# Kernel tuning notes

Hardware: AMD Instinct MI355X
Metric: run time of the kernel (lower is better)

Reference implementation:

```python
import jax, jax.numpy as jnp
import numpy as np
import math

B, S, H = 4, 2048, 1024
NE, NC, CD, OD = 4, 16, 64, 128  # num_experiments, num_exp_codes, exp_code_dim, outcome_dim
TAU, TEMP, EPS = 0.5, 0.07, 1e-5


def gelu(x):
    return jax.nn.gelu(x, approximate=False)


def layer_norm(x, g, b):
    m = x.mean(-1, keepdims=True)
    v = ((x - m) ** 2).mean(-1, keepdims=True)
    return (x - m) * jax.lax.rsqrt(v + EPS) * g + b


def setup_inputs() -> dict:
    key = jax.random.key(0)
    ks = jax.random.split(key, 24)
    lin = lambda k, i, o: jax.random.normal(k, (i, o), jnp.float32) * 0.02
    u = jax.random.uniform(ks[1], (B, NE, NC), minval=1e-6, maxval=1.0 - 1e-6)
    d = {
        "hidden_states": jax.random.normal(ks[0], (B, S, H), jnp.float32),
        "attention_mask": jnp.ones((B, S), jnp.int32),
        "gumbel_noise": -jnp.log(-jnp.log(u)),
        # context_pooler: Linear(H,H) + LayerNorm
        "cp_w": lin(ks[2], H, H), "cp_b": jnp.zeros(H), "cp_ln_g": jnp.ones(H), "cp_ln_b": jnp.zeros(H),
        # eph: Linear(H,H), Linear(H, NE*NC)
        "eph_w1": lin(ks[3], H, H), "eph_b1": jnp.zeros(H),
        "eph_w2": lin(ks[4], H, NE * NC), "eph_b2": jnp.zeros(NE * NC),
        "codebook": jax.random.normal(ks[5], (NC, CD), jnp.float32) * 0.02,
        # world_kernel: Linear(H+CD, 2H), Linear(2H, OD)
        "wk_w1": lin(ks[6], H + CD, 2 * H), "wk_b1": jnp.zeros(2 * H),
        "wk_w2": lin(ks[7], 2 * H, OD), "wk_b2": jnp.zeros(OD),
        "tp_w": lin(ks[8], H, OD),  # target_proj, no bias
        # film_proj: Linear(OD, 2H) + GELU
        "film_w": lin(ks[9], OD, 2 * H), "film_b": jnp.zeros(2 * H),
        "q_w": lin(ks[10], H, H), "q_b": jnp.zeros(H),
        "k_w": lin(ks[11], H, H), "k_b": jnp.zeros(H),
        "v_w": lin(ks[12], H, H), "v_b": jnp.zeros(H),
        "o_w": lin(ks[13], H, H), "o_b": jnp.zeros(H),
        "int_w": lin(ks[14], H, 4 * H), "int_b": jnp.zeros(4 * H),
        "out_w": lin(ks[15], 4 * H, H), "out_b": jnp.zeros(H),
        "ln_g": jnp.ones(H), "ln_b": jnp.zeros(H),
    }
    return d


def reference(hidden_states, attention_mask, gumbel_noise,
              cp_w, cp_b, cp_ln_g, cp_ln_b,
              eph_w1, eph_b1, eph_w2, eph_b2, codebook,
              wk_w1, wk_b1, wk_w2, wk_b2, tp_w, film_w, film_b,
              q_w, q_b, k_w, k_b, v_w, v_b, o_w, o_b,
              int_w, int_b, out_w, out_b, ln_g, ln_b):
    mask = attention_mask.astype(hidden_states.dtype)  # [B,S]
    # --- context pooling ---
    denom = mask.sum(1, keepdims=True) + 1e-8
    pooled = (hidden_states * mask[:, :, None]).sum(1) / denom  # [B,H]
    h_ctx = layer_norm(gelu(pooled @ cp_w + cp_b), cp_ln_g, cp_ln_b)
    # --- experiment proposal (gumbel-softmax, hard, tau=0.5) ---
    z_raw = gelu(h_ctx @ eph_w1 + eph_b1) @ eph_w2 + eph_b2
    z_logits = z_raw.reshape(B, NE, NC)
    y_soft = jax.nn.softmax((z_logits + gumbel_noise) / TAU, axis=-1)
    y_hard = jax.nn.one_hot(jnp.argmax(y_soft, -1), NC, dtype=y_soft.dtype)
    z_soft = y_hard - jax.lax.stop_gradient(y_soft) + y_soft  # straight-through
    z_codes = z_soft @ codebook  # [B,NE,CD]
    # --- world kernel ---
    h_rep = jnp.broadcast_to(h_ctx[:, None, :], (B, NE, H))
    h_wk = jnp.concatenate([h_rep, z_codes], -1)  # [B,NE,H+CD]
    outcome = gelu(h_wk @ wk_w1 + wk_b1) @ wk_w2 + wk_b2  # [B,NE,OD]
    # --- info gain (labels/plan_vector None branch) ---
    tv = h_ctx @ tp_w
    tv = tv / jnp.linalg.norm(tv, axis=-1, keepdims=True).clip(1e-12)
    on = outcome / jnp.linalg.norm(outcome, axis=-1, keepdims=True).clip(1e-12)
    info_gain = jnp.sum(on * tv[:, None, :], -1) / TEMP  # [B,NE]
    idx = jnp.argmax(info_gain, -1)  # [B]
    chosen = jnp.take_along_axis(outcome, idx[:, None, None], axis=1)[:, 0]  # [B,OD]
    # --- FiLM ---
    gb = gelu(chosen @ film_w + film_b)  # [B,2H]
    gamma, beta = gb[:, :H], gb[:, H:]
    fused = gamma[:, None, :] * hidden_states + beta[:, None, :]  # [B,S,H]
    # --- single-head attention ---
    q = fused @ q_w + q_b
    k = fused @ k_w + k_b
    v = fused @ v_w + v_b
    scores = jnp.einsum('bqd,bkd->bqk', q, k) / math.sqrt(H)
    scores = jnp.where(attention_mask[:, None, :] == 0, -jnp.inf, scores)
    attn = jax.nn.softmax(scores, axis=-1)
    attn_out = jnp.einsum('bqk,bkd->bqd', attn, v) @ o_w + o_b
    # --- FFN + residual + LN ---
    ff = gelu((attn_out + fused) @ int_w + int_b) @ out_w + out_b
    return layer_norm(ff + fused, ln_g, ln_b)
```

## Files before the change

### kernel.cpp

```cpp
#include <hip/hip_runtime.h>
#include <math.h>

#define DEVI __device__ __forceinline__

typedef unsigned short u16;
typedef __attribute__((ext_vector_type(4))) float f32x4;
typedef __attribute__((ext_vector_type(8))) short s16x8;
typedef __attribute__((ext_vector_type(4))) short s16x4;

constexpr int Bc = 4, Sc = 2048, Hc = 1024;
constexpr int NEc = 4, NCc = 16, CDc = 64, ODc = 128;
constexpr float TAUc = 0.5f, TEMPc = 0.07f, EPSc = 1e-5f;

DEVI float gelu_f(float x) { return 0.5f * x * (1.0f + erff(x * 0.7071067811865476f)); }

DEVI float bf2f(u16 u) { union { unsigned int i; float f; } v; v.i = ((unsigned int)u) << 16; return v.f; }
DEVI u16 f2bf(float f) {
  union { float f; unsigned int i; } v; v.f = f;
  unsigned int u = v.i;
  unsigned int r = (u + 0x7fffu + ((u >> 16) & 1u)) >> 16;
  return (u16)r;
}

DEVI float wred_sum(float v) {
  #pragma unroll
  for (int o = 32; o > 0; o >>= 1) v += __shfl_down(v, o);
  return v;
}
DEVI float wred_max(float v) {
  #pragma unroll
  for (int o = 32; o > 0; o >>= 1) v = fmaxf(v, __shfl_down(v, o));
  return v;
}

DEVI void gload16(const void* g, void* l) {
  __builtin_amdgcn_global_load_lds((const __attribute__((address_space(1))) void*)g,
                                   (__attribute__((address_space(3))) void*)l, 16, 0, 0);
}

template<int EPI>
__global__ __launch_bounds__(256, 3) void gemm_bt(
    const u16* __restrict__ A, long sAz, int lda,
    const u16* __restrict__ Bt, long sBz, int ldb,
    u16* __restrict__ C, long sCz, int ldc,
    const float* __restrict__ bias,
    const u16* __restrict__ resid, long sRz,
    float scale, int M, int N, int K)
{
  const int bz = blockIdx.z;
  A += (long)bz * sAz; Bt += (long)bz * sBz; C += (long)bz * sCz;
  if (EPI & 4) resid += (long)bz * sRz;

  const int nTn = N >> 7;
  const int tm = blockIdx.x / nTn, tn = blockIdx.x % nTn;
  const int tid = threadIdx.x;
  const int wid = tid >> 6, lane = tid & 63;
  const int wr = wid >> 1, wc = wid & 1;
  const int l15 = lane & 15, l4 = lane >> 4;

  __shared__ u16 As[128 * 32];
  __shared__ u16 Bs[128 * 32];

  f32x4 acc[4][4];
  #pragma unroll
  for (int i = 0; i < 4; ++i)
    #pragma unroll
    for (int j = 0; j < 4; ++j) acc[i][j] = f32x4{0.f, 0.f, 0.f, 0.f};

  const int srow = (wid << 5) + (lane >> 2);
  const int scol = (lane & 3) << 3;
  const u16* aS = A + (long)(tm * 128 + srow) * lda + scol;
  const u16* bS = Bt + (long)(tn * 128 + srow) * ldb + scol;
  const long aStep16 = (long)16 * lda;
  const long bStep16 = (long)16 * ldb;
  u16* aD = &As[wid * 32 * 32];
  u16* bD = &Bs[wid * 32 * 32];

  for (int k0 = 0; k0 < K; k0 += 32) {
    gload16(aS, aD);
    gload16(aS + aStep16, aD + 16 * 32);
    gload16(bS, bD);
    gload16(bS + bStep16, bD + 16 * 32);
    __syncthreads();
    s16x8 af[4], bfr[4];
    #pragma unroll
    for (int i = 0; i < 4; ++i) {
      const int row = (wr << 6) + (i << 4) + l15;
      af[i] = *(const s16x8*)&As[(row << 5) + (l4 << 3)];
    }
    #pragma unroll
    for (int j = 0; j < 4; ++j) {
      const int col = (wc << 6) + (j << 4) + l15;
      bfr[j] = *(const s16x8*)&Bs[(col << 5) + (l4 << 3)];
    }
    #pragma unroll
    for (int i = 0; i < 4; ++i)
      #pragma unroll
      for (int j = 0; j < 4; ++j)
        acc[i][j] = __builtin_amdgcn_mfma_f32_16x16x32_bf16(af[i], bfr[j], acc[i][j], 0, 0, 0);
    __syncthreads();
    aS += 32; bS += 32;
  }

  #pragma unroll
  for (int j = 0; j < 4; ++j) {
    const int col = tn * 128 + (wc << 6) + (j << 4) + l15;
    const float bv = (EPI & 1) ? bias[col] : 0.f;
    #pragma unroll
    for (int i = 0; i < 4; ++i) {
      const int row0 = tm * 128 + (wr << 6) + (i << 4) + (l4 << 2);
      float vv[4];
      #pragma unroll
      for (int r = 0; r < 4; ++r) {
        float v = acc[i][j][r] * scale + bv;
        if (EPI & 2) v = gelu_f(v);
        if (EPI & 4) v += bf2f(resid[(long)(row0 + r) * ldc + col]);
        vv[r] = v;
      }
      if (EPI & 8) {
        s16x4 pk = { (short)f2bf(vv[0]), (short)f2bf(vv[1]), (short)f2bf(vv[2]), (short)f2bf(vv[3]) };
        *(s16x4*)&C[(long)col * ldc + row0] = pk;
      } else {
        #pragma unroll
        for (int r = 0; r < 4; ++r) C[(long)(row0 + r) * ldc + col] = f2bf(vv[r]);
      }
    }
  }
}

__global__ void transpose_w_k(const float* __restrict__ in, u16* __restrict__ out, int K, int N) {
  __shared__ float t[32][33];
  const int n0 = blockIdx.x << 5, k0 = blockIdx.y << 5;
  const int tx = threadIdx.x, ty = threadIdx.y;
  #pragma unroll
  for (int i = 0; i < 32; i += 8)
    t[ty + i][tx] = in[(long)(k0 + ty + i) * N + n0 + tx];
  __syncthreads();
  #pragma unroll
  for (int i = 0; i < 32; i += 8)
    out[(long)(n0 + ty + i) * K + k0 + tx] = f2bf(t[tx][ty + i]);
}

__global__ void transpose_w4_k(const float* __restrict__ w0, const float* __restrict__ w1,
                               const float* __restrict__ w2, const float* __restrict__ w3,
                               u16* __restrict__ o0, u16* __restrict__ o1,
                               u16* __restrict__ o2, u16* __restrict__ o3) {
  const int z = blockIdx.z;
  const float* in = (z == 0) ? w0 : (z == 1) ? w1 : (z == 2) ? w2 : w3;
  u16* out = (z == 0) ? o0 : (z == 1) ? o1 : (z == 2) ? o2 : o3;
  __shared__ float t[32][33];
  const int n0 = blockIdx.x << 5, k0 = blockIdx.y << 5;
  const int tx = threadIdx.x, ty = threadIdx.y;
  #pragma unroll
  for (int i = 0; i < 32; i += 8)
    t[ty + i][tx] = in[(long)(k0 + ty + i) * Hc + n0 + tx];
  __syncthreads();
  #pragma unroll
  for (int i = 0; i < 32; i += 8)
    out[(long)(n0 + ty + i) * Hc + k0 + tx] = f2bf(t[tx][ty + i]);
}

__global__ void pool_partial_k(const float* __restrict__ hs, const int* __restrict__ mask,
                               float* __restrict__ part) {
  const int h = (blockIdx.x << 8) + threadIdx.x;
  const int c = blockIdx.y, b = blockIdx.z;
  const int s0 = c * (Sc / 16);
  float acc = 0.f;
  for (int i = 0; i < Sc / 16; ++i) {
    const int s = s0 + i;
    acc += hs[((long)b * Sc + s) * Hc + h] * (float)mask[b * Sc + s];
  }
  part[((b << 4) + c) * Hc + h] = acc;
}

__global__ void pool_final_k(const float* __restrict__ part, const int* __restrict__ mask,
                             float* __restrict__ pooled) {
  const int b = blockIdx.x;
  __shared__ float red[4];
  __shared__ float denom_s;
  float d = 0.f;
  for (int i = threadIdx.x; i < Sc; i += 256) d += (float)mask[b * Sc + i];
  d = wred_sum(d);
  if ((threadIdx.x & 63) == 0) red[threadIdx.x >> 6] = d;
  __syncthreads();
  if (threadIdx.x == 0) denom_s = red[0] + red[1] + red[2] + red[3] + 1e-8f;
  __syncthreads();
  const float inv = 1.f / denom_s;
  for (int h = threadIdx.x; h < Hc; h += 256) {
    float s = 0.f;
    #pragma unroll
    for (int c = 0; c < 16; ++c) s += part[((b << 4) + c) * Hc + h];
    pooled[b * Hc + h] = s * inv;
  }
}

template<int R>
__global__ void mrow_part_k(const float* __restrict__ in, const float* __restrict__ W,
                            float* __restrict__ part, int K, int N) {
  const int t = threadIdx.x;
  const int jj = t & 31;
  const int j = (blockIdx.x << 5) + jj;
  const int ks = t >> 5;
  const int nchunk = gridDim.y;
  const int Kc = K / (nchunk << 3);
  const int k0 = ((blockIdx.y << 3) + ks) * Kc;
  float acc[R];
  #pragma unroll
  for (int r = 0; r < R; ++r) acc[r] = 0.f;
  for (int k = k0; k < k0 + Kc; ++k) {
    const float wv = W[(long)k * N + j];
    #pragma unroll
    for (int r = 0; r < R; ++r) acc[r] = fmaf(in[r * K + k], wv, acc[r]);
  }
  __shared__ float sm[8][R][32];
  #pragma unroll
  for (int r = 0; r < R; ++r) sm[ks][r][jj] = acc[r];
  __syncthreads();
  for (int idx = t; idx < R * 32; idx += 256) {
    const int r = idx >> 5, j2 = idx & 31;
    float s = 0.f;
    #pragma unroll
    for (int q = 0; q < 8; ++q) s += sm[q][r][j2];
    part[(long)(blockIdx.y * R + r) * N + (blockIdx.x << 5) + j2] = s;
  }
}

template<bool GELU>
__global__ void mrow_reduce_k(const float* __restrict__ part, const float* __restrict__ bias,
                              float* __restrict__ out, int N, int R, int nchunk) {
  const int idx = (blockIdx.x << 8) + threadIdx.x;
  if (idx >= R * N) return;
  const int r = idx / N, j = idx - r * N;
  float s = 0.f;
  for (int c = 0; c < nchunk; ++c) s += part[(long)(c * R + r) * N + j];
  if (bias) s += bias[j];
  if (GELU) s = gelu_f(s);
  out[(long)r * N + j] = s;
}

__global__ void ln_rows_k(float* __restrict__ x, const float* __restrict__ g,
                          const float* __restrict__ b) {
  const long base = (long)blockIdx.x * Hc;
  __shared__ float red[4];
  float v[4]; float s = 0.f;
  #pragma unroll
  for (int i = 0; i < 4; ++i) { v[i] = x[base + threadIdx.x + (i << 8)]; s += v[i]; }
  s = wred_sum(s);
  if ((threadIdx.x & 63) == 0) red[threadIdx.x >> 6] = s;
  __syncthreads();
  const float mean = (red[0] + red[1] + red[2] + red[3]) * (1.f / Hc);
  float q = 0.f;
  #pragma unroll
  for (int i = 0; i < 4; ++i) { const float d2 = v[i] - mean; q += d2 * d2; }
  __syncthreads();
  q = wred_sum(q);
  if ((threadIdx.x & 63) == 0) red[threadIdx.x >> 6] = q;
  __syncthreads();
  const float var = (red[0] + red[1] + red[2] + red[3]) * (1.f / Hc);
  const float inv = rsqrtf(var + EPSc);
  #pragma unroll
  for (int i = 0; i < 4; ++i) {
    const int col = threadIdx.x + (i << 8);
    x[base + col] = (v[i] - mean) * inv * g[col] + b[col];
  }
}

__global__ void gumbel_k(const float* __restrict__ z, const float* __restrict__ gn,
                         const float* __restrict__ cb, float* __restrict__ zcodes) {
  const int b = blockIdx.x, t = threadIdx.x;
  if (t >= NEc) return;
  const float* zp = z + b * (NEc * NCc) + t * NCc;
  const float* gp = gn + (b * NEc + t) * NCc;
  int best = 0; float bv = -3.4e38f;
  for (int c2 = 0; c2 < NCc; ++c2) {
    const float val = (zp[c2] + gp[c2]) * (1.f / TAUc);
    if (val > bv) { bv = val; best = c2; }
  }
  for (int d2 = 0; d2 < CDc; ++d2)
    zcodes[(b * NEc + t) * CDc + d2] = cb[best * CDc + d2];
}

__global__ void build_hwk_k(const float* __restrict__ hctx, const float* __restrict__ zcodes,
                            float* __restrict__ hwk) {
  const int r = blockIdx.x;
  const int b = r >> 2;
  for (int i = threadIdx.x; i < Hc + CDc; i += 256)
    hwk[r * (Hc + CDc) + i] = (i < Hc) ? hctx[b * Hc + i] : zcodes[r * CDc + (i - Hc)];
}

__global__ void select_k(const float* __restrict__ tv, const float* __restrict__ outc,
                         float* __restrict__ chosen) {
  const int b = blockIdx.x, t = threadIdx.x;
  __shared__ float red[2];
  __shared__ float ig[NEc];
  __shared__ int bestIdx;
  const float x = tv[b * ODc + t];
  float ss = wred_sum(x * x);
  if ((t & 63) == 0) red[t >> 6] = ss;
  __syncthreads();
  float nrm = fmaxf(sqrtf(red[0] + red[1]), 1e-12f);
  const float tvn = x / nrm;
  __syncthreads();
  for (int ne = 0; ne < NEc; ++ne) {
    const float o = outc[(b * NEc + ne) * ODc + t];
    float a = wred_sum(o * o);
    float d2 = wred_sum(o * tvn);
    if ((t & 63) == 0) red[t >> 6] = a;
    __syncthreads();
    const float no = sqrtf(red[0] + red[1]);
    __syncthreads();
    if ((t & 63) == 0) red[t >> 6] = d2;
    __syncthreads();
    const float dd = red[0] + red[1];
    if (t == 0) ig[ne] = dd / fmaxf(no, 1e-12f) * (1.f / TEMPc);
    __syncthreads();
  }
  if (t == 0) {
    int bi = 0; float bvv = ig[0];
    for (int ne = 1; ne < NEc; ++ne) if (ig[ne] > bvv) { bvv = ig[ne]; bi = ne; }
    bestIdx = bi;
  }
  __syncthreads();
  chosen[b * ODc + t] = outc[(b * NEc + bestIdx) * ODc + t];
}

__global__ void fuse_k(const float* __restrict__ hs, const float* __restrict__ gb,
                       u16* __restrict__ fused) {
  const long i = (((long)blockIdx.x << 8) + threadIdx.x) << 2;
  const int h = (int)(i & (Hc - 1));
  const int b = (int)(i >> 21);
  const float4 xv = *(const float4*)(hs + i);
  const float* gp = gb + b * 2048;
  s16x4 pk = { (short)f2bf(fmaf(gp[h + 0], xv.x, gp[Hc + h + 0])),
               (short)f2bf(fmaf(gp[h + 1], xv.y, gp[Hc + h + 1])),
               (short)f2bf(fmaf(gp[h + 2], xv.z, gp[Hc + h + 2])),
               (short)f2bf(fmaf(gp[h + 3], xv.w, gp[Hc + h + 3])) };
  *(s16x4*)(fused + i) = pk;
}

__global__ void softmax_k(u16* __restrict__ sc, const int* __restrict__ mask) {
  const long base = (long)blockIdx.x * Sc;
  const int b = blockIdx.x / Sc;
  __shared__ float red[4];
  float x[8];
  float mx = -3.0e38f;
  #pragma unroll
  for (int i = 0; i < 8; ++i) {
    const int col = threadIdx.x + (i << 8);
    float v = bf2f(sc[base + col]);
    if (mask[b * Sc + col] == 0) v = -3.0e38f;
    x[i] = v;
    mx = fmaxf(mx, v);
  }
  mx = wred_max(mx);
  if ((threadIdx.x & 63) == 0) red[threadIdx.x >> 6] = mx;
  __syncthreads();
  mx = fmaxf(fmaxf(red[0], red[1]), fmaxf(red[2], red[3]));
  float sum = 0.f;
  #pragma unroll
  for (int i = 0; i < 8; ++i) { x[i] = __expf(x[i] - mx); sum += x[i]; }
  __syncthreads();
  sum = wred_sum(sum);
  if ((threadIdx.x & 63) == 0) red[threadIdx.x >> 6] = sum;
  __syncthreads();
  const float inv = 1.f / (red[0] + red[1] + red[2] + red[3]);
  #pragma unroll
  for (int i = 0; i < 8; ++i)
    sc[base + threadIdx.x + (i << 8)] = f2bf(x[i] * inv);
}

__global__ void final_ln_k(const u16* __restrict__ ff, const u16* __restrict__ fused,
                           const float* __restrict__ g, const float* __restrict__ b,
                           float* __restrict__ out) {
  const long base = (long)blockIdx.x * Hc;
  __shared__ float red[4];
  float v[4]; float s = 0.f;
  #pragma unroll
  for (int i = 0; i < 4; ++i) {
    const int col = threadIdx.x + (i << 8);
    v[i] = bf2f(ff[base + col]) + bf2f(fused[base + col]);
    s += v[i];
  }
  s = wred_sum(s);
  if ((threadIdx.x & 63) == 0) red[threadIdx.x >> 6] = s;
  __syncthreads();
  const float mean = (red[0] + red[1] + red[2] + red[3]) * (1.f / Hc);
  float q = 0.f;
  #pragma unroll
  for (int i = 0; i < 4; ++i) { const float d2 = v[i] - mean; q += d2 * d2; }
  __syncthreads();
  q = wred_sum(q);
  if ((threadIdx.x & 63) == 0) red[threadIdx.x >> 6] = q;
  __syncthreads();
  const float var = (red[0] + red[1] + red[2] + red[3]) * (1.f / Hc);
  const float inv = rsqrtf(var + EPSc);
  #pragma unroll
  for (int i = 0; i < 4; ++i) {
    const int col = threadIdx.x + (i << 8);
    out[base + col] = (v[i] - mean) * inv * g[col] + b[col];
  }
}

extern "C" void kernel_launch(void* const* d_in, const int* in_sizes, int n_in,
                              void* d_out, int out_size, void* d_ws, size_t ws_size,
                              hipStream_t stream) {
  const float* hs       = (const float*)d_in[0];
  const int*   amask    = (const int*)d_in[1];
  const float* gn       = (const float*)d_in[2];
  const float* cp_w     = (const float*)d_in[3];
  const float* cp_b     = (const float*)d_in[4];
  const float* cp_ln_g  = (const float*)d_in[5];
  const float* cp_ln_b  = (const float*)d_in[6];
  const float* eph_w1   = (const float*)d_in[7];
  const float* eph_b1   = (const float*)d_in[8];
  const float* eph_w2   = (const float*)d_in[9];
  const float* eph_b2   = (const float*)d_in[10];
  const float* codebook = (const float*)d_in[11];
  const float* wk_w1    = (const float*)d_in[12];
  const float* wk_b1    = (const float*)d_in[13];
  const float* wk_w2    = (const float*)d_in[14];
  const float* wk_b2    = (const float*)d_in[15];
  const float* tp_w     = (const float*)d_in[16];
  const float* film_w   = (const float*)d_in[17];
  const float* film_b   = (const float*)d_in[18];
  const float* q_w      = (const float*)d_in[19];
  const float* q_bias   = (const float*)d_in[20];
  const float* k_w      = (const float*)d_in[21];
  const float* k_bias   = (const float*)d_in[22];
  const float* v_w      = (const float*)d_in[23];
  const float* v_bias   = (const float*)d_in[24];
  const float* o_w      = (const float*)d_in[25];
  const float* o_bias   = (const float*)d_in[26];
  const float* int_w    = (const float*)d_in[27];
  const float* int_b    = (const float*)d_in[28];
  const float* out_w    = (const float*)d_in[29];
  const float* out_b    = (const float*)d_in[30];
  const float* ln_g     = (const float*)d_in[31];
  const float* ln_b     = (const float*)d_in[32];
  float* outp = (float*)d_out;

  char* w = (char*)d_ws;
  auto alloc = [&](size_t bytes) -> char* {
    char* p = w; w += (bytes + 255) & ~(size_t)255; return p;
  };
  float* part    = (float*)alloc((size_t)Bc * 16 * Hc * 4);
  float* pooled  = (float*)alloc((size_t)Bc * Hc * 4);
  float* hctx    = (float*)alloc((size_t)Bc * Hc * 4);
  float* t1      = (float*)alloc((size_t)Bc * Hc * 4);
  float* zlog    = (float*)alloc((size_t)Bc * 64 * 4);
  float* zcodes  = (float*)alloc((size_t)Bc * NEc * CDc * 4);
  float* hwk     = (float*)alloc((size_t)16 * (Hc + CDc) * 4);
  float* wkt1    = (float*)alloc((size_t)16 * 2048 * 4);
  float* outcome = (float*)alloc((size_t)16 * ODc * 4);
  float* tvb     = (float*)alloc((size_t)Bc * ODc * 4);
  float* chosen  = (float*)alloc((size_t)Bc * ODc * 4);
  float* gb      = (float*)alloc((size_t)Bc * 2048 * 4);
  float* lin_part= (float*)alloc((size_t)1024 * 1024);
  u16* qT    = (u16*)alloc((size_t)Hc * Hc * 2);
  u16* kT    = (u16*)alloc((size_t)Hc * Hc * 2);
  u16* vTw   = (u16*)alloc((size_t)Hc * Hc * 2);
  u16* oT    = (u16*)alloc((size_t)Hc * Hc * 2);
  u16* intT  = (u16*)alloc((size_t)Hc * 4096 * 2);
  u16* outT  = (u16*)alloc((size_t)Hc * 4096 * 2);
  u16* fused = (u16*)alloc((size_t)8192 * Hc * 2);
  u16* qact  = (u16*)alloc((size_t)8192 * Hc * 2);
  u16* kact  = (u16*)alloc((size_t)8192 * Hc * 2);
  u16* scores= (u16*)alloc((size_t)Bc * Sc * Sc * 2);
  u16* vTact = (u16*)alloc((size_t)8192 * Hc * 2);
  u16* attn  = (u16*)alloc((size_t)8192 * Hc * 2);
  u16* h1    = (u16*)alloc((size_t)8192 * Hc * 2);
  u16* mid = qact;
  u16* ffo = attn;

  if ((size_t)(w - (char*)d_ws) > ws_size) return;

  const dim3 tb32(32, 8);
  transpose_w4_k<<<dim3(32, 32, 4), tb32, 0, stream>>>(q_w, k_w, v_w, o_w, qT, kT, vTw, oT);
  transpose_w_k<<<dim3(4096 / 32, Hc / 32), tb32, 0, stream>>>(int_w, intT, Hc, 4096);
  transpose_w_k<<<dim3(Hc / 32, 4096 / 32), tb32, 0, stream>>>(out_w, outT, 4096, Hc);

  pool_partial_k<<<dim3(Hc / 256, 16, Bc), 256, 0, stream>>>(hs, amask, part);
  pool_final_k<<<Bc, 256, 0, stream>>>(part, amask, pooled);

  mrow_part_k<4><<<dim3(32, 8), 256, 0, stream>>>(pooled, cp_w, lin_part, Hc, Hc);
  mrow_reduce_k<true><<<16, 256, 0, stream>>>(lin_part, cp_b, hctx, Hc, 4, 8);
  ln_rows_k<<<Bc, 256, 0, stream>>>(hctx, cp_ln_g, cp_ln_b);
  mrow_part_k<4><<<dim3(32, 8), 256, 0, stream>>>(hctx, eph_w1, lin_part, Hc, Hc);
  mrow_reduce_k<true><<<16, 256, 0, stream>>>(lin_part, eph_b1, t1, Hc, 4, 8);
  mrow_part_k<4><<<dim3(2, 16), 256, 0, stream>>>(t1, eph_w2, lin_part, Hc, 64);
  mrow_reduce_k<false><<<1, 256, 0, stream>>>(lin_part, eph_b2, zlog, 64, 4, 16);
  gumbel_k<<<Bc, 64, 0, stream>>>(zlog, gn, codebook, zcodes);
  build_hwk_k<<<Bc * NEc, 256, 0, stream>>>(hctx, zcodes, hwk);
  mrow_part_k<16><<<dim3(64, 8), 256, 0, stream>>>(hwk, wk_w1, lin_part, Hc + CDc, 2048);
  mrow_reduce_k<true><<<128, 256, 0, stream>>>(lin_part, wk_b1, wkt1, 2048, 16, 8);
  mrow_part_k<16><<<dim3(4, 32), 256, 0, stream>>>(wkt1, wk_w2, lin_part, 2048, ODc);
  mrow_reduce_k<false><<<8, 256, 0, stream>>>(lin_part, wk_b2, outcome, ODc, 16, 32);
  mrow_part_k<4><<<dim3(4, 8), 256, 0, stream>>>(hctx, tp_w, lin_part, Hc, ODc);
  mrow_reduce_k<false><<<2, 256, 0, stream>>>(lin_part, nullptr, tvb, ODc, 4, 8);
  select_k<<<Bc, 128, 0, stream>>>(tvb, outcome, chosen);
  mrow_part_k<4><<<dim3(64, 2), 256, 0, stream>>>(chosen, film_w, lin_part, ODc, 2048);
  mrow_reduce_k<true><<<32, 256, 0, stream>>>(lin_part, film_b, gb, 2048, 4, 2);
  fuse_k<<<8192, 256, 0, stream>>>(hs, gb, fused);

  gemm_bt<1><<<dim3(512), 256, 0, stream>>>(fused, 0, Hc, qT, 0, Hc, qact, 0, Hc,
                                            q_bias, nullptr, 0, 1.f, 8192, Hc, Hc);
  gemm_bt<1><<<dim3(512), 256, 0, stream>>>(fused, 0, Hc, kT, 0, Hc, kact, 0, Hc,
                                            k_bias, nullptr, 0, 1.f, 8192, Hc, Hc);
  gemm_bt<9><<<dim3(512), 256, 0, stream>>>(fused, 0, Hc, vTw, 0, Hc, vTact, 0, 8192,
                                            v_bias, nullptr, 0, 1.f, 8192, Hc, Hc);
  gemm_bt<0><<<dim3(256, 1, Bc), 256, 0, stream>>>(qact, (long)Sc * Hc, Hc,
                                                   kact, (long)Sc * Hc, Hc,
                                                   scores, (long)Sc * Sc, Sc,
                                                   nullptr, nullptr, 0, 0.03125f, Sc, Sc, Hc);
  softmax_k<<<Bc * Sc, 256, 0, stream>>>(scores, amask);
  gemm_bt<0><<<dim3(128, 1, Bc), 256, 0, stream>>>(scores, (long)Sc * Sc, Sc,
                                                   vTact, (long)Sc, 8192,
                                                   attn, (long)Sc * Hc, Hc,
                                                   nullptr, nullptr, 0, 1.f, Sc, Hc, Sc);
  gemm_bt<5><<<dim3(512), 256, 0, stream>>>(attn, 0, Hc, oT, 0, Hc, h1, 0, Hc,
                                            o_bias, fused, 0, 1.f, 8192, Hc, Hc);
  gemm_bt<3><<<dim3(2048), 256, 0, stream>>>(h1, 0, Hc, intT, 0, Hc, mid, 0, 4096,
                                             int_b, nullptr, 0, 1.f, 8192, 4096, Hc);
  gemm_bt<1><<<dim3(512), 256, 0, stream>>>(mid, 0, 4096, outT, 0, 4096, ffo, 0, Hc,
                                            out_b, nullptr, 0, 1.f, 8192, Hc, 4096);
  final_ln_k<<<Bc * Sc, 256, 0, stream>>>(ffo, fused, ln_g, ln_b, outp);
}
```

Baseline: 596.6 us.

## Merge Q/K projections, swizzle GEMM block order, and stage epilogue through LDS

Fuses the Q and K projection GEMMs into one N=2048 GEMM. This relies on qT and kT lying next to each other in the workspace and on a concatenated bias buffer. It remaps block IDs so consecutive workgroups spread across output tiles for better cache locality. It also rewrites the GEMM epilogue to stage results in shared memory and write 16-byte coalesced stores, including the transposed V output and the residual add. The costs are extra LDS use, extra barriers, and a dependence on the workspace layout: qT and kT are allocated one after the other, each 1024x1024 bf16, and 256-byte alignment holds, so they are contiguous.

```diff
diff --git a/kernel.cpp b/kernel.cpp
--- a/kernel.cpp
+++ b/kernel.cpp
@@ -51,15 +51,20 @@
   A += (long)bz * sAz; Bt += (long)bz * sBz; C += (long)bz * sCz;
   if (EPI & 4) resid += (long)bz * sRz;
 
+  int bid = blockIdx.x;
+  const int nwg = gridDim.x;
+  if ((nwg & 7) == 0) bid = ((bid & 7) * (nwg >> 3)) + (bid >> 3);
+
   const int nTn = N >> 7;
-  const int tm = blockIdx.x / nTn, tn = blockIdx.x % nTn;
+  const int tm = bid / nTn, tn = bid % nTn;
   const int tid = threadIdx.x;
   const int wid = tid >> 6, lane = tid & 63;
   const int wr = wid >> 1, wc = wid & 1;
   const int l15 = lane & 15, l4 = lane >> 4;
 
-  __shared__ u16 As[128 * 32];
-  __shared__ u16 Bs[128 * 32];
+  __shared__ u16 smem[9216];
+  u16* As = smem;
+  u16* Bs = smem + 4096;
 
   f32x4 acc[4][4];
   #pragma unroll
@@ -102,28 +107,79 @@
     aS += 32; bS += 32;
   }
 
-  #pragma unroll
-  for (int j = 0; j < 4; ++j) {
-    const int col = tn * 128 + (wc << 6) + (j << 4) + l15;
-    const float bv = (EPI & 1) ? bias[col] : 0.f;
-    #pragma unroll
-    for (int i = 0; i < 4; ++i) {
-      const int row0 = tm * 128 + (wr << 6) + (i << 4) + (l4 << 2);
-      float vv[4];
+  if (!(EPI & 8)) {
+    u16 (*Cs)[128] = (u16(*)[128])smem;
+    #pragma unroll
+    for (int p = 0; p < 2; ++p) {
+      if (wr == p) {
+        #pragma unroll
+        for (int j = 0; j < 4; ++j) {
+          const int c = (wc << 6) + (j << 4) + l15;
+          const float bv = (EPI & 1) ? bias[tn * 128 + c] : 0.f;
+          #pragma unroll
+          for (int i = 0; i < 4; ++i) {
+            const int lr = (i << 4) + (l4 << 2);
+            #pragma unroll
+            for (int r = 0; r < 4; ++r) {
+              float v = acc[i][j][r] * scale + bv;
+              if (EPI & 2) v = gelu_f(v);
+              Cs[lr + r][c] = f2bf(v);
+            }
+          }
+        }
+      }
+      __syncthreads();
       #pragma unroll
-      for (int r = 0; r < 4; ++r) {
-        float v = acc[i][j][r] * scale + bv;
-        if (EPI & 2) v = gelu_f(v);
-        if (EPI & 4) v += bf2f(resid[(long)(row0 + r) * ldc + col]);
-        vv[r] = v;
+      for (int it = 0; it < 4; ++it) {
+        const int row = (tid >> 4) + (it << 4);
+        const int chunk = tid & 15;
+        const long Gr = tm * 128 + (p << 6) + row;
+        const int col0 = tn * 128 + (chunk << 3);
+        s16x8 cv = *(s16x8*)&Cs[row][chunk << 3];
+        if (EPI & 4) {
+          const s16x8 rv = *(const s16x8*)&resid[Gr * ldc + col0];
+          #pragma unroll
+          for (int e = 0; e < 8; ++e)
+            cv[e] = (short)f2bf(bf2f((u16)cv[e]) + bf2f((u16)rv[e]));
+        }
+        *(s16x8*)&C[Gr * ldc + col0] = cv;
       }
-      if (EPI & 8) {
-        s16x4 pk = { (short)f2bf(vv[0]), (short)f2bf(vv[1]), (short)f2bf(vv[2]), (short)f2bf(vv[3]) };
-        *(s16x4*)&C[(long)col * ldc + row0] = pk;
-      } else {
+      if (p == 0) __syncthreads();
+    }
+  } else {
+    u16 (*Ct)[136] = (u16(*)[136])smem;
+    #pragma unroll
+    for (int p = 0; p < 2; ++p) {
+      if (wc == p) {
         #pragma unroll
-        for (int r = 0; r < 4; ++r) C[(long)(row0 + r) * ldc + col] = f2bf(vv[r]);
+        for (int j = 0; j < 4; ++j) {
+          const int lc = (j << 4) + l15;
+          const float bv = (EPI & 1) ? bias[tn * 128 + (p << 6) + lc] : 0.f;
+          #pragma unroll
+          for (int i = 0; i < 4; ++i) {
+            const int row_lo = (wr << 6) + (i << 4) + (l4 << 2);
+            s16x4 pk;
+            #pragma unroll
+            for (int r = 0; r < 4; ++r) {
+              float v = acc[i][j][r] * scale + bv;
+              if (EPI & 2) v = gelu_f(v);
+              pk[r] = (short)f2bf(v);
+            }
+            *(s16x4*)&Ct[lc][row_lo] = pk;
+          }
+        }
       }
+      __syncthreads();
+      #pragma unroll
+      for (int it = 0; it < 4; ++it) {
+        const int lc = (tid >> 4) + (it << 4);
+        const int chunk = tid & 15;
+        const long Gc = tn * 128 + (p << 6) + lc;
+        const int col0 = tm * 128 + (chunk << 3);
+        s16x8 cv = *(s16x8*)&Ct[lc][chunk << 3];
+        *(s16x8*)&C[Gc * ldc + col0] = cv;
+      }
+      if (p == 0) __syncthreads();
     }
   }
 }
@@ -158,6 +214,12 @@
   #pragma unroll
   for (int i = 0; i < 32; i += 8)
     out[(long)(n0 + ty + i) * Hc + k0 + tx] = f2bf(t[tx][ty + i]);
+}
+
+__global__ void concat_bias_k(const float* __restrict__ a, const float* __restrict__ b,
+                              float* __restrict__ o) {
+  const int i = (blockIdx.x << 8) + threadIdx.x;
+  o[i] = (i < Hc) ? a[i] : b[i - Hc];
 }
 
 __global__ void pool_partial_k(const float* __restrict__ hs, const int* __restrict__ mask,
@@ -456,6 +518,7 @@
   float* chosen  = (float*)alloc((size_t)Bc * ODc * 4);
   float* gb      = (float*)alloc((size_t)Bc * 2048 * 4);
   float* lin_part= (float*)alloc((size_t)1024 * 1024);
+  float* qk_bias = (float*)alloc((size_t)2048 * 4);
   u16* qT    = (u16*)alloc((size_t)Hc * Hc * 2);
   u16* kT    = (u16*)alloc((size_t)Hc * Hc * 2);
   u16* vTw   = (u16*)alloc((size_t)Hc * Hc * 2);
@@ -463,13 +526,12 @@
   u16* intT  = (u16*)alloc((size_t)Hc * 4096 * 2);
   u16* outT  = (u16*)alloc((size_t)Hc * 4096 * 2);
   u16* fused = (u16*)alloc((size_t)8192 * Hc * 2);
-  u16* qact  = (u16*)alloc((size_t)8192 * Hc * 2);
-  u16* kact  = (u16*)alloc((size_t)8192 * Hc * 2);
+  u16* qkact = (u16*)alloc((size_t)8192 * 2048 * 2);
   u16* scores= (u16*)alloc((size_t)Bc * Sc * Sc * 2);
   u16* vTact = (u16*)alloc((size_t)8192 * Hc * 2);
   u16* attn  = (u16*)alloc((size_t)8192 * Hc * 2);
   u16* h1    = (u16*)alloc((size_t)8192 * Hc * 2);
-  u16* mid = qact;
+  u16* mid = qkact;
   u16* ffo = attn;
 
   if ((size_t)(w - (char*)d_ws) > ws_size) return;
@@ -478,6 +540,7 @@
   transpose_w4_k<<<dim3(32, 32, 4), tb32, 0, stream>>>(q_w, k_w, v_w, o_w, qT, kT, vTw, oT);
   transpose_w_k<<<dim3(4096 / 32, Hc / 32), tb32, 0, stream>>>(int_w, intT, Hc, 4096);
   transpose_w_k<<<dim3(Hc / 32, 4096 / 32), tb32, 0, stream>>>(out_w, outT, 4096, Hc);
+  concat_bias_k<<<8, 256, 0, stream>>>(q_bias, k_bias, qk_bias);
 
   pool_partial_k<<<dim3(Hc / 256, 16, Bc), 256, 0, stream>>>(hs, amask, part);
   pool_final_k<<<Bc, 256, 0, stream>>>(part, amask, pooled);
@@ -502,14 +565,12 @@
   mrow_reduce_k<true><<<32, 256, 0, stream>>>(lin_part, film_b, gb, 2048, 4, 2);
   fuse_k<<<8192, 256, 0, stream>>>(hs, gb, fused);
 
-  gemm_bt<1><<<dim3(512), 256, 0, stream>>>(fused, 0, Hc, qT, 0, Hc, qact, 0, Hc,
-                                            q_bias, nullptr, 0, 1.f, 8192, Hc, Hc);
-  gemm_bt<1><<<dim3(512), 256, 0, stream>>>(fused, 0, Hc, kT, 0, Hc, kact, 0, Hc,
-                                            k_bias, nullptr, 0, 1.f, 8192, Hc, Hc);
+  gemm_bt<1><<<dim3(1024), 256, 0, stream>>>(fused, 0, Hc, qT, 0, Hc, qkact, 0, 2048,
+                                             qk_bias, nullptr, 0, 1.f, 8192, 2048, Hc);
   gemm_bt<9><<<dim3(512), 256, 0, stream>>>(fused, 0, Hc, vTw, 0, Hc, vTact, 0, 8192,
                                             v_bias, nullptr, 0, 1.f, 8192, Hc, Hc);
-  gemm_bt<0><<<dim3(256, 1, Bc), 256, 0, stream>>>(qact, (long)Sc * Hc, Hc,
-                                                   kact, (long)Sc * Hc, Hc,
+  gemm_bt<0><<<dim3(256, 1, Bc), 256, 0, stream>>>(qkact, (long)Sc * 2048, 2048,
+                                                   qkact + 1024, (long)Sc * 2048, 2048,
                                                    scores, (long)Sc * Sc, Sc,
                                                    nullptr, nullptr, 0, 0.03125f, Sc, Sc, Hc);
   softmax_k<<<Bc * Sc, 256, 0, stream>>>(scores, amask);
```

Measured after the change: 560.2 us, median of 2. 1.06x faster.
